# Optimization experiments

Hardware: AMD Instinct MI355X
Metric: run time of the kernel (lower is better)

## Reference

```python
import jax, jax.numpy as jnp
import numpy as np

GORDER = 8
IN_DIM = 32768
CLASSES = 10


def setup_inputs() -> dict:
    key = jax.random.key(0)
    k1, k2 = jax.random.split(key)
    x = jax.random.normal(k1, (2048, IN_DIM), dtype=jnp.float32)
    weight = jax.random.normal(k2, (CLASSES, IN_DIM), dtype=jnp.float32)
    radius = jnp.ones((1,), dtype=jnp.float32)
    return {"x": x, "weight": weight, "radius": radius}


def reference(x, weight, radius):
    # theta = 2*pi/gorder * value
    c = jnp.float32(2.0 * np.pi / GORDER)
    tx = c * x            # (B, K)
    tw = c * weight       # (O, K)
    # GroupSim: radius * sum_i cos(tw[o,i] - tx[b,i])
    #         = radius * (cos(tx) @ cos(tw)^T + sin(tx) @ sin(tw)^T)
    sims = jnp.einsum('bk,ok->bo', jnp.cos(tx), jnp.cos(tw)) \
         + jnp.einsum('bk,ok->bo', jnp.sin(tx), jnp.sin(tw))
    sims = radius[0] * sims
    return sims * jnp.float32(1.0 / IN_DIM ** 0.5)
```

## Files before the change

### kernel.cpp

```cpp
#include <hip/hip_runtime.h>


typedef _Float16 half2_t __attribute__((ext_vector_type(2)));
typedef _Float16 half8_t __attribute__((ext_vector_type(8)));
typedef float f32x4 __attribute__((ext_vector_type(4)));

#define K_DIM 32768
#define B_DIM 2048
#define O_DIM 10
#define NWIN 2048
#define KCH 64
#define WPC (NWIN / KCH)
#define ITERS (WPC / 2)
#define MTILES (B_DIM / 64)
#define THREADS 256
#define INV_SQRT_K 0.005524271728019903f


__device__ __forceinline__ half2_t pack_cs(float c, float s) {
    return __builtin_bit_cast(half2_t, __builtin_amdgcn_cvt_pkrtz(c, s));
}

__device__ __forceinline__ half8_t afrag(float4 xc) {
    const float* xf = (const float*)&xc;
    uint4 au;
    unsigned u[4];
    #pragma unroll
    for (int j = 0; j < 4; ++j) {
        float rr = xf[j] * 0.125f;
        u[j] = __builtin_bit_cast(unsigned,
                   pack_cs(__builtin_amdgcn_cosf(rr),
                           __builtin_amdgcn_sinf(rr)));
    }
    au.x = u[0]; au.y = u[1]; au.z = u[2]; au.w = u[3];
    return __builtin_bit_cast(half8_t, au);
}

__global__ void wtab_kernel(const float* __restrict__ w,
                            uint4* __restrict__ wtab) {
    int gid = blockIdx.x * THREADS + threadIdx.x;
    int t = gid >> 6, l = gid & 63;
    int o = l & 15, kg = l >> 4;
    int k = t * 16 + kg * 4;
    uint4 v; v.x = v.y = v.z = v.w = 0u;
    if (o < O_DIM) {
        const float4 wv = *(const float4*)(w + (size_t)o * K_DIM + k);
        const float* wp = (const float*)&wv;
        unsigned u[4];
        #pragma unroll
        for (int j = 0; j < 4; ++j) {
            float rr = wp[j] * 0.125f;
            u[j] = __builtin_bit_cast(unsigned,
                       pack_cs(__builtin_amdgcn_cosf(rr),
                               __builtin_amdgcn_sinf(rr)));
        }
        v.x = u[0]; v.y = u[1]; v.z = u[2]; v.w = u[3];
    }
    wtab[gid] = v;
}

__global__ __launch_bounds__(THREADS) void gsim_mfma(
        const float* __restrict__ x,
        const uint4* __restrict__ wtab,
        float* __restrict__ part) {
    const int bid = blockIdx.x;
    const int mt = bid & (MTILES - 1);
    const int kc = bid >> 5;
    const int t = threadIdx.x;
    const int wave = t >> 6, lane = t & 63;
    const int o = lane & 15, kg = lane >> 4;

    const int row = mt * 64 + wave * 16 + o;
    const int t0 = kc * WPC;
    const float4* xp = (const float4*)x + ((size_t)row * (K_DIM / 4) + t0 * 4 + kg);
    const uint4* bp = wtab + (size_t)t0 * 64 + lane;

    f32x4 acc = {0.f, 0.f, 0.f, 0.f};

    float4 xc0 = xp[0], xc1 = xp[4];
    uint4  bc0 = bp[0], bc1 = bp[64];

    #pragma unroll 1
    for (int i = 0; i < ITERS; ++i) {
        const int ni = (i + 1 < ITERS) ? (i + 1) : i;
        float4 xn0 = xp[ni * 8],       xn1 = xp[ni * 8 + 4];
        uint4  bn0 = bp[ni * 128],     bn1 = bp[ni * 128 + 64];

        half8_t a0 = afrag(xc0);
        acc = __builtin_amdgcn_mfma_f32_16x16x32_f16(
                  a0, __builtin_bit_cast(half8_t, bc0), acc, 0, 0, 0);
        half8_t a1 = afrag(xc1);
        acc = __builtin_amdgcn_mfma_f32_16x16x32_f16(
                  a1, __builtin_bit_cast(half8_t, bc1), acc, 0, 0, 0);

        xc0 = xn0; xc1 = xn1; bc0 = bn0; bc1 = bn1;
    }

    const int rbase = mt * 64 + wave * 16 + kg * 4;
    float* pp = part + ((size_t)kc * B_DIM + rbase) * 16 + o;
    #pragma unroll
    for (int reg = 0; reg < 4; ++reg)
        pp[(size_t)reg * 16] = acc[reg];
}

__global__ void finalize_kernel(const float* __restrict__ part,
                                const float* __restrict__ radius,
                                float* __restrict__ out) {
    int gid = blockIdx.x * THREADS + threadIdx.x;
    int b = gid >> 4, o = gid & 15;
    if (o >= O_DIM) return;
    float s = 0.f;
    #pragma unroll 8
    for (int kc = 0; kc < KCH; ++kc)
        s += part[(size_t)kc * (B_DIM * 16) + gid];
    out[(size_t)b * O_DIM + o] = s * radius[0] * INV_SQRT_K;
}

extern "C" void kernel_launch(void* const* d_in, const int* in_sizes, int n_in,
                              void* d_out, int out_size, void* d_ws, size_t ws_size,
                              hipStream_t stream) {
    const float* x      = (const float*)d_in[0];
    const float* w      = (const float*)d_in[1];
    const float* radius = (const float*)d_in[2];
    float* out = (float*)d_out;

    uint4* wtab = (uint4*)d_ws;
    float* part = (float*)((char*)d_ws + (size_t)NWIN * 64 * 16);

    hipLaunchKernelGGL(wtab_kernel, dim3(NWIN * 64 / THREADS), dim3(THREADS),
                       0, stream, w, wtab);
    hipLaunchKernelGGL(gsim_mfma, dim3(MTILES * KCH), dim3(THREADS),
                       0, stream, x, wtab, part);
    hipLaunchKernelGGL(finalize_kernel, dim3(B_DIM * 16 / THREADS), dim3(THREADS),
                       0, stream, part, radius, out);
}
```

Before: 60.26 us.

## Stage x tiles through swizzled LDS with register double-buffered global loads

Replaces the per-lane strided float4 loads of x with coalesced row-contiguous global loads into a double-buffered register set. These are written to an XOR-swizzled shared-memory tile and then read back in MFMA fragment order. The goal is to improve global memory coalescing and keep more loads in flight to hide latency. The cost is two barriers per step, extra LDS traffic, and higher register pressure from the 16 float4 buffers, which may reduce occupancy.

Result: slower. 145.8 us (+141.9%).

```diff
diff --git a/kernel.cpp b/kernel.cpp
--- a/kernel.cpp
+++ b/kernel.cpp
@@ -11,7 +11,8 @@
 #define NWIN 2048
 #define KCH 64
 #define WPC (NWIN / KCH)
-#define ITERS (WPC / 2)
+#define BK 128
+#define STEPS (WPC / 8)
 #define MTILES (B_DIM / 64)
 #define THREADS 256
 #define INV_SQRT_K 0.005524271728019903f
@@ -63,6 +64,8 @@
         const float* __restrict__ x,
         const uint4* __restrict__ wtab,
         float* __restrict__ part) {
+    __shared__ float xtile[64 * BK];
+
     const int bid = blockIdx.x;
     const int mt = bid & (MTILES - 1);
     const int kc = bid >> 5;
@@ -70,30 +73,47 @@
     const int wave = t >> 6, lane = t & 63;
     const int o = lane & 15, kg = lane >> 4;
 
-    const int row = mt * 64 + wave * 16 + o;
-    const int t0 = kc * WPC;
-    const float4* xp = (const float4*)x + ((size_t)row * (K_DIM / 4) + t0 * 4 + kg);
-    const uint4* bp = wtab + (size_t)t0 * 64 + lane;
+    const int srow = t >> 5;
+    const int sc16 = t & 31;
+    const int ldsw0 = srow * 512 + ((sc16 ^ srow) << 4);
+    const float* gbase = x + ((size_t)(mt * 64 + srow) * K_DIM) + kc * 512 + sc16 * 4;
+
+    const int rowf = wave * 16 + o;
+    const int lds_rbase = rowf * 512;
+    const int o7 = o & 7;
+
+    const uint4* bp = wtab + (size_t)(kc * WPC) * 64 + lane;
 
     f32x4 acc = {0.f, 0.f, 0.f, 0.f};
+    float4 gbuf[2][8];
 
-    float4 xc0 = xp[0], xc1 = xp[4];
-    uint4  bc0 = bp[0], bc1 = bp[64];
+    #pragma unroll
+    for (int i = 0; i < 8; ++i)
+        gbuf[0][i] = *(const float4*)(gbase + (size_t)i * 8 * K_DIM);
 
-    #pragma unroll 1
-    for (int i = 0; i < ITERS; ++i) {
-        const int ni = (i + 1 < ITERS) ? (i + 1) : i;
-        float4 xn0 = xp[ni * 8],       xn1 = xp[ni * 8 + 4];
-        uint4  bn0 = bp[ni * 128],     bn1 = bp[ni * 128 + 64];
+    #pragma unroll
+    for (int s = 0; s < STEPS; ++s) {
+        __syncthreads();
+        #pragma unroll
+        for (int i = 0; i < 8; ++i)
+            *(float4*)((char*)xtile + i * 4096 + ldsw0) = gbuf[s & 1][i];
+        if (s + 1 < STEPS) {
+            #pragma unroll
+            for (int i = 0; i < 8; ++i)
+                gbuf[(s + 1) & 1][i] =
+                    *(const float4*)(gbase + (s + 1) * BK + (size_t)i * 8 * K_DIM);
+        }
+        __syncthreads();
 
-        half8_t a0 = afrag(xc0);
-        acc = __builtin_amdgcn_mfma_f32_16x16x32_f16(
-                  a0, __builtin_bit_cast(half8_t, bc0), acc, 0, 0, 0);
-        half8_t a1 = afrag(xc1);
-        acc = __builtin_amdgcn_mfma_f32_16x16x32_f16(
-                  a1, __builtin_bit_cast(half8_t, bc1), acc, 0, 0, 0);
-
-        xc0 = xn0; xc1 = xn1; bc0 = bn0; bc1 = bn1;
+        #pragma unroll
+        for (int tw = 0; tw < 8; ++tw) {
+            uint4 bc = bp[(size_t)(s * 8 + tw) * 64];
+            float4 xv = *(const float4*)((const char*)xtile + lds_rbase
+                            + ((((tw << 2) + kg) ^ o7) << 4));
+            half8_t a = afrag(xv);
+            acc = __builtin_amdgcn_mfma_f32_16x16x32_f16(
+                      a, __builtin_bit_cast(half8_t, bc), acc, 0, 0, 0);
+        }
     }
 
     const int rbase = mt * 64 + wave * 16 + kg * 4;
```

## Remap K layout so each lane loads 64 contiguous bytes per group, deepen prefetch

Applied to the files above, without the earlier changes.

Changes the K-index permutation so each lane reads four consecutive float4s (64 contiguous bytes) of x per group, with the weight table reordered to match. The main loop now processes four MFMAs per iteration, prefetching four x and four weight fragments at a time. The aim is better memory coalescing and more loads in flight to hide latency on the bandwidth-bound x stream, at the cost of more registers.

After: 62.69 us. +4.0%, slower.

```diff
diff --git a/kernel.cpp b/kernel.cpp
--- a/kernel.cpp
+++ b/kernel.cpp
@@ -11,7 +11,7 @@
 #define NWIN 2048
 #define KCH 64
 #define WPC (NWIN / KCH)
-#define ITERS (WPC / 2)
+#define GROUPS (WPC / 4)
 #define MTILES (B_DIM / 64)
 #define THREADS 256
 #define INV_SQRT_K 0.005524271728019903f
@@ -41,7 +41,7 @@
     int gid = blockIdx.x * THREADS + threadIdx.x;
     int t = gid >> 6, l = gid & 63;
     int o = l & 15, kg = l >> 4;
-    int k = t * 16 + kg * 4;
+    int k = (t >> 2) * 64 + kg * 16 + (t & 3) * 4;
     uint4 v; v.x = v.y = v.z = v.w = 0u;
     if (o < O_DIM) {
         const float4 wv = *(const float4*)(w + (size_t)o * K_DIM + k);
@@ -71,29 +71,33 @@
     const int o = lane & 15, kg = lane >> 4;
 
     const int row = mt * 64 + wave * 16 + o;
-    const int t0 = kc * WPC;
-    const float4* xp = (const float4*)x + ((size_t)row * (K_DIM / 4) + t0 * 4 + kg);
-    const uint4* bp = wtab + (size_t)t0 * 64 + lane;
+    const float4* xp = (const float4*)(x + (size_t)row * K_DIM + kc * 512 + kg * 16);
+    const uint4* bp = wtab + (size_t)(kc * WPC) * 64 + lane;
 
     f32x4 acc = {0.f, 0.f, 0.f, 0.f};
 
-    float4 xc0 = xp[0], xc1 = xp[4];
-    uint4  bc0 = bp[0], bc1 = bp[64];
+    float4 xc0 = xp[0], xc1 = xp[1], xc2 = xp[2], xc3 = xp[3];
+    uint4  bc0 = bp[0], bc1 = bp[64], bc2 = bp[128], bc3 = bp[192];
 
     #pragma unroll 1
-    for (int i = 0; i < ITERS; ++i) {
-        const int ni = (i + 1 < ITERS) ? (i + 1) : i;
-        float4 xn0 = xp[ni * 8],       xn1 = xp[ni * 8 + 4];
-        uint4  bn0 = bp[ni * 128],     bn1 = bp[ni * 128 + 64];
+    for (int g = 0; g < GROUPS; ++g) {
+        const int ng = (g + 1 < GROUPS) ? (g + 1) : g;
+        float4 xn0 = xp[ng * 16],     xn1 = xp[ng * 16 + 1],
+               xn2 = xp[ng * 16 + 2], xn3 = xp[ng * 16 + 3];
+        uint4  bn0 = bp[(size_t)ng * 256],       bn1 = bp[(size_t)ng * 256 + 64],
+               bn2 = bp[(size_t)ng * 256 + 128], bn3 = bp[(size_t)ng * 256 + 192];
 
-        half8_t a0 = afrag(xc0);
         acc = __builtin_amdgcn_mfma_f32_16x16x32_f16(
-                  a0, __builtin_bit_cast(half8_t, bc0), acc, 0, 0, 0);
-        half8_t a1 = afrag(xc1);
+                  afrag(xc0), __builtin_bit_cast(half8_t, bc0), acc, 0, 0, 0);
         acc = __builtin_amdgcn_mfma_f32_16x16x32_f16(
-                  a1, __builtin_bit_cast(half8_t, bc1), acc, 0, 0, 0);
+                  afrag(xc1), __builtin_bit_cast(half8_t, bc1), acc, 0, 0, 0);
+        acc = __builtin_amdgcn_mfma_f32_16x16x32_f16(
+                  afrag(xc2), __builtin_bit_cast(half8_t, bc2), acc, 0, 0, 0);
+        acc = __builtin_amdgcn_mfma_f32_16x16x32_f16(
+                  afrag(xc3), __builtin_bit_cast(half8_t, bc3), acc, 0, 0, 0);
 
-        xc0 = xn0; xc1 = xn1; bc0 = bn0; bc1 = bn1;
+        xc0 = xn0; xc1 = xn1; xc2 = xn2; xc3 = xn3;
+        bc0 = bn0; bc1 = bn1; bc2 = bn2; bc3 = bn3;
     }
 
     const int rbase = mt * 64 + wave * 16 + kg * 4;
```
